# Performance work log

Measured on AMD Instinct MI355X. Metric: run time of the kernel, lower is better.

The kernel has to match this reference:

```python
import jax, jax.numpy as jnp
import numpy as np

B, CD, GD, F, H = 8192, 512, 512, 1024, 8
HD = F // H
EPS = 1e-5  # torch LayerNorm default


def _layernorm(x, g, b):
    m = x.mean(-1, keepdims=True)
    v = ((x - m) ** 2).mean(-1, keepdims=True)
    return (x - m) / jnp.sqrt(v + EPS) * g + b


def setup_inputs() -> dict:
    key = jax.random.key(0)
    ks = jax.random.split(key, 24)
    s = lambda fan_in: 1.0 / np.sqrt(fan_in)
    return {
        "cnn_embed": jax.random.normal(ks[0], (B, CD), jnp.float32),
        "gnn_embed": jax.random.normal(ks[1], (B, GD), jnp.float32),
        # projections (torch Linear: y = x @ W.T + b)
        "cnn_w": jax.random.normal(ks[2], (F, CD), jnp.float32) * s(CD),
        "cnn_b": jax.random.normal(ks[3], (F,), jnp.float32) * s(CD),
        "gnn_w": jax.random.normal(ks[4], (F, GD), jnp.float32) * s(GD),
        "gnn_b": jax.random.normal(ks[5], (F,), jnp.float32) * s(GD),
        # layernorms
        "ln1_g": jnp.ones((F,), jnp.float32),
        "ln1_b": jnp.zeros((F,), jnp.float32),
        "ln2_g": jnp.ones((F,), jnp.float32),
        "ln2_b": jnp.zeros((F,), jnp.float32),
        # MultiheadAttention packed in-proj + out-proj
        "attn_in_w": jax.random.normal(ks[6], (3 * F, F), jnp.float32) * s(F),
        "attn_in_b": jnp.zeros((3 * F,), jnp.float32),
        "attn_out_w": jax.random.normal(ks[7], (F, F), jnp.float32) * s(F),
        "attn_out_b": jnp.zeros((F,), jnp.float32),
        # gate MLP: Linear(2F->F) GELU Linear(F->2) Softmax
        "gate_w1": jax.random.normal(ks[8], (F, 2 * F), jnp.float32) * s(2 * F),
        "gate_b1": jnp.zeros((F,), jnp.float32),
        "gate_w2": jax.random.normal(ks[9], (2, F), jnp.float32) * s(F),
        "gate_b2": jnp.zeros((2,), jnp.float32),
        # out_proj: Linear(F->F) GELU (dropout is identity in eval)
        "proj_w": jax.random.normal(ks[10], (F, F), jnp.float32) * s(F),
        "proj_b": jnp.zeros((F,), jnp.float32),
    }


def reference(cnn_embed, gnn_embed, cnn_w, cnn_b, gnn_w, gnn_b,
              ln1_g, ln1_b, ln2_g, ln2_b,
              attn_in_w, attn_in_b, attn_out_w, attn_out_b,
              gate_w1, gate_b1, gate_w2, gate_b2, proj_w, proj_b):
    c = _layernorm(cnn_embed @ cnn_w.T + cnn_b, ln1_g, ln1_b)  # [B,F]
    g = _layernorm(gnn_embed @ gnn_w.T + gnn_b, ln2_g, ln2_b)  # [B,F]
    combined = jnp.stack([c, g], axis=1)  # [B,2,F]

    # self-attention over the 2-token "sequence" (q=k=v=combined)
    qkv = combined @ attn_in_w.T + attn_in_b  # [B,2,3F]
    q, k, v = jnp.split(qkv, 3, axis=-1)
    split_heads = lambda t: t.reshape(B, 2, H, HD).transpose(0, 2, 1, 3)  # [B,H,2,HD]
    q, k, v = split_heads(q), split_heads(k), split_heads(v)
    scores = jnp.einsum("bhqd,bhkd->bhqk", q, k) / np.sqrt(HD)  # [B,H,2,2]
    attn = jax.nn.softmax(scores, axis=-1)
    o = jnp.einsum("bhqk,bhkd->bhqd", attn, v)  # [B,H,2,HD]
    o = o.transpose(0, 2, 1, 3).reshape(B, 2, F)
    attn_out = o @ attn_out_w.T + attn_out_b  # [B,2,F]

    c_attn = attn_out[:, 0]
    g_attn = attn_out[:, 1]
    gate_in = jnp.concatenate([c_attn, g_attn], axis=-1)  # [B,2F]
    gate_h = jax.nn.gelu(gate_in @ gate_w1.T + gate_b1, approximate=False)
    gate_weights = jax.nn.softmax(gate_h @ gate_w2.T + gate_b2, axis=-1)  # [B,2]

    fused = gate_weights[:, 0:1] * c_attn + gate_weights[:, 1:2] * g_attn
    fused = jax.nn.gelu(fused @ proj_w.T + proj_b, approximate=False)  # dropout=eval identity
    return fused, gate_weights
```

## Files before the change

kernel.cpp:

```cpp
#include <hip/hip_runtime.h>
#include <hip/hip_bf16.h>
#include <math.h>

typedef short short8 __attribute__((ext_vector_type(8)));
typedef float floatx4 __attribute__((ext_vector_type(4)));

__device__ __forceinline__ float bf2f(ushort u) {
    union { unsigned int i; float f; } v; v.i = ((unsigned int)u) << 16; return v.f;
}
__device__ __forceinline__ ushort f2bf(float f) {
    union { float f; unsigned int i; } v; v.f = f;
    unsigned int x = v.i;
    unsigned int lsb = (x >> 16) & 1u;
    x += 0x7fffu + lsb;
    return (ushort)(x >> 16);
}
__device__ __forceinline__ float gelu_f(float x) {
    return 0.5f * x * (1.0f + erff(x * 0.7071067811865475f));
}
__device__ __forceinline__ void store4(ushort* p, float a, float b, float c, float d) {
    ushort4 o; o.x = f2bf(a); o.y = f2bf(b); o.z = f2bf(c); o.w = f2bf(d);
    *(ushort4*)p = o;
}
__device__ __forceinline__ void store4(float* p, float a, float b, float c, float d) {
    *(float4*)p = make_float4(a, b, c, d);
}

struct CvtDesc {
    const float* in[8];
    ushort* out[8];
    int nblk[8];
};
__global__ __launch_bounds__(256) void cvt_all_kernel(CvtDesc d) {
    int b = blockIdx.x;
    int s = 0;
    int off = b;
    while (off >= d.nblk[s]) { off -= d.nblk[s]; s++; }
    int i = off * 1024 + threadIdx.x * 4;
    float4 v = *(const float4*)(d.in[s] + i);
    ushort4 o;
    o.x = f2bf(v.x); o.y = f2bf(v.y); o.z = f2bf(v.z); o.w = f2bf(v.w);
    *(ushort4*)(d.out[s] + i) = o;
}

template<int ACT, typename TOUT>
__global__ __launch_bounds__(256) void gemm_bt(const ushort* __restrict__ A, int lda,
                                               const ushort* __restrict__ W,
                                               const float* __restrict__ bias,
                                               TOUT* __restrict__ C, int ldc,
                                               int M, int N, int K) {
    __shared__ ushort lsA[128 * 32];
    __shared__ ushort lsB[128 * 32];
    const int t = threadIdx.x;
    const int w = t >> 6, l = t & 63;
    const int q = l >> 4, r16 = l & 15;
    const int wm = (w >> 1) * 64, wn = (w & 1) * 64;
    const int m0 = blockIdx.y * 128, n0 = blockIdx.x * 128;

    floatx4 acc[4][4];
#pragma unroll
    for (int i = 0; i < 4; i++)
#pragma unroll
        for (int j = 0; j < 4; j++) acc[i][j] = (floatx4){0.f, 0.f, 0.f, 0.f};

    const int kc = (t & 3) * 8;

    for (int kt = 0; kt < K; kt += 32) {
        __syncthreads();
#pragma unroll
        for (int rr = 0; rr < 2; ++rr) {
            int c = rr * 256 + t;
            int row = c >> 2;
            const ushort* ga = A + (size_t)(m0 + row) * lda + kt + kc;
            const ushort* gb = W + (size_t)(n0 + row) * K + kt + kc;
            __builtin_amdgcn_global_load_lds((const __attribute__((address_space(1))) void*)ga,
                                             (__attribute__((address_space(3))) void*)&lsA[c * 8],
                                             16, 0, 0);
            __builtin_amdgcn_global_load_lds((const __attribute__((address_space(1))) void*)gb,
                                             (__attribute__((address_space(3))) void*)&lsB[c * 8],
                                             16, 0, 0);
        }
        __syncthreads();
        short8 af[4], bfr[4];
#pragma unroll
        for (int i = 0; i < 4; i++) af[i]  = *(const short8*)&lsA[(wm + i * 16 + r16) * 32 + q * 8];
#pragma unroll
        for (int j = 0; j < 4; j++) bfr[j] = *(const short8*)&lsB[(wn + j * 16 + r16) * 32 + q * 8];
#pragma unroll
        for (int i = 0; i < 4; i++)
#pragma unroll
            for (int j = 0; j < 4; j++)
                acc[i][j] = __builtin_amdgcn_mfma_f32_16x16x32_bf16(bfr[j], af[i], acc[i][j], 0, 0, 0);
    }

#pragma unroll
    for (int j = 0; j < 4; j++) {
        const int col = n0 + wn + j * 16 + q * 4;
        const float4 bv = *(const float4*)(bias + col);
#pragma unroll
        for (int i = 0; i < 4; i++) {
            const int row = m0 + wm + i * 16 + r16;
            float v0 = acc[i][j][0] + bv.x;
            float v1 = acc[i][j][1] + bv.y;
            float v2 = acc[i][j][2] + bv.z;
            float v3 = acc[i][j][3] + bv.w;
            if (ACT == 1) { v0 = gelu_f(v0); v1 = gelu_f(v1); v2 = gelu_f(v2); v3 = gelu_f(v3); }
            store4(&C[(size_t)row * ldc + col], v0, v1, v2, v3);
        }
    }
}

__global__ __launch_bounds__(256) void ln_kernel(ushort* __restrict__ comb,
                                                 const float* __restrict__ g1, const float* __restrict__ b1,
                                                 const float* __restrict__ g2, const float* __restrict__ b2) {
    int row = blockIdx.x;
    int s = row & 1;
    const float* g = s ? g2 : g1;
    const float* bb = s ? b2 : b1;
    ushort* p = comb + (size_t)row * 1024;
    int t = threadIdx.x;
    ushort4 u = *(const ushort4*)(p + t * 4);
    float x0 = bf2f(u.x), x1 = bf2f(u.y), x2 = bf2f(u.z), x3 = bf2f(u.w);
    float sum = x0 + x1 + x2 + x3;
    float ss = x0 * x0 + x1 * x1 + x2 * x2 + x3 * x3;
#pragma unroll
    for (int off = 32; off; off >>= 1) {
        sum += __shfl_xor(sum, off);
        ss  += __shfl_xor(ss, off);
    }
    __shared__ float sm[8];
    int wv = t >> 6, l = t & 63;
    if (l == 0) { sm[wv * 2] = sum; sm[wv * 2 + 1] = ss; }
    __syncthreads();
    sum = sm[0] + sm[2] + sm[4] + sm[6];
    ss  = sm[1] + sm[3] + sm[5] + sm[7];
    float mean = sum * (1.0f / 1024.0f);
    float var  = ss * (1.0f / 1024.0f) - mean * mean;
    float rstd = rsqrtf(var + 1e-5f);
    float4 gv = *(const float4*)(g + t * 4);
    float4 bv = *(const float4*)(bb + t * 4);
    ushort4 o;
    o.x = f2bf((x0 - mean) * rstd * gv.x + bv.x);
    o.y = f2bf((x1 - mean) * rstd * gv.y + bv.y);
    o.z = f2bf((x2 - mean) * rstd * gv.z + bv.z);
    o.w = f2bf((x3 - mean) * rstd * gv.w + bv.w);
    *(ushort4*)(p + t * 4) = o;
}

__global__ __launch_bounds__(256) void attn_kernel(ushort* __restrict__ qkv) {
    int wid = blockIdx.x * 4 + (threadIdx.x >> 6);
    int l = threadIdx.x & 63;
    int b = wid >> 3, h = wid & 7;
    ushort* base0 = qkv + (size_t)(b * 2) * 3072 + h * 128 + 2 * l;
    ushort* base1 = base0 + 3072;
    ushort2 uq0 = *(const ushort2*)(base0);
    ushort2 uq1 = *(const ushort2*)(base1);
    ushort2 uk0 = *(const ushort2*)(base0 + 1024);
    ushort2 uk1 = *(const ushort2*)(base1 + 1024);
    ushort2 uv0 = *(const ushort2*)(base0 + 2048);
    ushort2 uv1 = *(const ushort2*)(base1 + 2048);
    float q0a = bf2f(uq0.x), q0b = bf2f(uq0.y);
    float q1a = bf2f(uq1.x), q1b = bf2f(uq1.y);
    float k0a = bf2f(uk0.x), k0b = bf2f(uk0.y);
    float k1a = bf2f(uk1.x), k1b = bf2f(uk1.y);
    float v0a = bf2f(uv0.x), v0b = bf2f(uv0.y);
    float v1a = bf2f(uv1.x), v1b = bf2f(uv1.y);
    float p00 = q0a * k0a + q0b * k0b;
    float p01 = q0a * k1a + q0b * k1b;
    float p10 = q1a * k0a + q1b * k0b;
    float p11 = q1a * k1a + q1b * k1b;
#pragma unroll
    for (int off = 32; off; off >>= 1) {
        p00 += __shfl_xor(p00, off);
        p01 += __shfl_xor(p01, off);
        p10 += __shfl_xor(p10, off);
        p11 += __shfl_xor(p11, off);
    }
    const float sc = 0.08838834764831845f;
    p00 *= sc; p01 *= sc; p10 *= sc; p11 *= sc;
    float m0 = fmaxf(p00, p01), m1 = fmaxf(p10, p11);
    float e00 = expf(p00 - m0), e01 = expf(p01 - m0);
    float e10 = expf(p10 - m1), e11 = expf(p11 - m1);
    float i0 = 1.0f / (e00 + e01), i1 = 1.0f / (e10 + e11);
    float a00 = e00 * i0, a01 = e01 * i0;
    float a10 = e10 * i1, a11 = e11 * i1;
    ushort2 o0, o1;
    o0.x = f2bf(a00 * v0a + a01 * v1a);
    o0.y = f2bf(a00 * v0b + a01 * v1b);
    o1.x = f2bf(a10 * v0a + a11 * v1a);
    o1.y = f2bf(a10 * v0b + a11 * v1b);
    *(ushort2*)(base0) = o0;
    *(ushort2*)(base1) = o1;
}

__global__ __launch_bounds__(256) void gate2_kernel(const ushort* __restrict__ gate_h,
                                                    const float* __restrict__ w2, const float* __restrict__ b2,
                                                    const ushort* __restrict__ attn_out,
                                                    ushort* __restrict__ fused_pre,
                                                    float* __restrict__ gw_out) {
    int b = blockIdx.x;
    int t = threadIdx.x;
    const ushort* hp = gate_h + (size_t)b * 1024;
    ushort4 u = *(const ushort4*)(hp + t * 4);
    float4 w0 = *(const float4*)(w2 + t * 4);
    float4 w1 = *(const float4*)(w2 + 1024 + t * 4);
    float h0 = bf2f(u.x), h1 = bf2f(u.y), h2 = bf2f(u.z), h3 = bf2f(u.w);
    float p0 = h0 * w0.x + h1 * w0.y + h2 * w0.z + h3 * w0.w;
    float p1 = h0 * w1.x + h1 * w1.y + h2 * w1.z + h3 * w1.w;
#pragma unroll
    for (int off = 32; off; off >>= 1) {
        p0 += __shfl_xor(p0, off);
        p1 += __shfl_xor(p1, off);
    }
    __shared__ float sm[8];
    __shared__ float sgw[2];
    int wv = t >> 6, l = t & 63;
    if (l == 0) { sm[wv * 2] = p0; sm[wv * 2 + 1] = p1; }
    __syncthreads();
    if (t == 0) {
        float d0 = sm[0] + sm[2] + sm[4] + sm[6] + b2[0];
        float d1 = sm[1] + sm[3] + sm[5] + sm[7] + b2[1];
        float mx = fmaxf(d0, d1);
        float e0 = expf(d0 - mx), e1 = expf(d1 - mx);
        float inv = 1.0f / (e0 + e1);
        sgw[0] = e0 * inv; sgw[1] = e1 * inv;
        gw_out[b * 2] = e0 * inv;
        gw_out[b * 2 + 1] = e1 * inv;
    }
    __syncthreads();
    float g0 = sgw[0], g1 = sgw[1];
    const ushort* ca = attn_out + (size_t)b * 2048;
    ushort* fp = fused_pre + (size_t)b * 1024;
    ushort4 uc = *(const ushort4*)(ca + t * 4);
    ushort4 ug = *(const ushort4*)(ca + 1024 + t * 4);
    ushort4 o;
    o.x = f2bf(g0 * bf2f(uc.x) + g1 * bf2f(ug.x));
    o.y = f2bf(g0 * bf2f(uc.y) + g1 * bf2f(ug.y));
    o.z = f2bf(g0 * bf2f(uc.z) + g1 * bf2f(ug.z));
    o.w = f2bf(g0 * bf2f(uc.w) + g1 * bf2f(ug.w));
    *(ushort4*)(fp + t * 4) = o;
}

#define OFF_A_CNN  0u
#define OFF_A_GNN  8388608u
#define OFF_W_CNN  16777216u
#define OFF_W_GNN  17825792u
#define OFF_W_QKV  18874368u
#define OFF_W_AO   25165824u
#define OFF_W_G1   27262976u
#define OFF_W_PJ   31457280u
#define OFF_COMB   33554432u
#define OFF_QKV    67108864u
#define OFF_AO     167772160u

extern "C" void kernel_launch(void* const* d_in, const int* in_sizes, int n_in,
                              void* d_out, int out_size, void* d_ws, size_t ws_size,
                              hipStream_t stream) {
    const float* cnn_embed  = (const float*)d_in[0];
    const float* gnn_embed  = (const float*)d_in[1];
    const float* cnn_w      = (const float*)d_in[2];
    const float* cnn_b      = (const float*)d_in[3];
    const float* gnn_w      = (const float*)d_in[4];
    const float* gnn_b      = (const float*)d_in[5];
    const float* ln1_g      = (const float*)d_in[6];
    const float* ln1_b      = (const float*)d_in[7];
    const float* ln2_g      = (const float*)d_in[8];
    const float* ln2_b      = (const float*)d_in[9];
    const float* attn_in_w  = (const float*)d_in[10];
    const float* attn_in_b  = (const float*)d_in[11];
    const float* attn_out_w = (const float*)d_in[12];
    const float* attn_out_b = (const float*)d_in[13];
    const float* gate_w1    = (const float*)d_in[14];
    const float* gate_b1    = (const float*)d_in[15];
    const float* gate_w2    = (const float*)d_in[16];
    const float* gate_b2    = (const float*)d_in[17];
    const float* proj_w     = (const float*)d_in[18];
    const float* proj_b     = (const float*)d_in[19];

    char* ws = (char*)d_ws;
    ushort* a_cnn  = (ushort*)(ws + OFF_A_CNN);
    ushort* a_gnn  = (ushort*)(ws + OFF_A_GNN);
    ushort* w_cnn  = (ushort*)(ws + OFF_W_CNN);
    ushort* w_gnn  = (ushort*)(ws + OFF_W_GNN);
    ushort* w_qkv  = (ushort*)(ws + OFF_W_QKV);
    ushort* w_ao   = (ushort*)(ws + OFF_W_AO);
    ushort* w_g1   = (ushort*)(ws + OFF_W_G1);
    ushort* w_pj   = (ushort*)(ws + OFF_W_PJ);
    ushort* comb   = (ushort*)(ws + OFF_COMB);
    ushort* qkv    = (ushort*)(ws + OFF_QKV);
    ushort* ao     = (ushort*)(ws + OFF_AO);
    ushort* gate_h    = (ushort*)(ws + OFF_COMB);
    ushort* fused_pre = (ushort*)(ws + OFF_COMB + 16777216u);

    float* out_f  = (float*)d_out;
    float* gw_out = out_f + 8192 * 1024;

    CvtDesc cd;
    cd.in[0] = cnn_embed;  cd.out[0] = a_cnn; cd.nblk[0] = 4096;
    cd.in[1] = gnn_embed;  cd.out[1] = a_gnn; cd.nblk[1] = 4096;
    cd.in[2] = cnn_w;      cd.out[2] = w_cnn; cd.nblk[2] = 512;
    cd.in[3] = gnn_w;      cd.out[3] = w_gnn; cd.nblk[3] = 512;
    cd.in[4] = attn_in_w;  cd.out[4] = w_qkv; cd.nblk[4] = 3072;
    cd.in[5] = attn_out_w; cd.out[5] = w_ao;  cd.nblk[5] = 1024;
    cd.in[6] = gate_w1;    cd.out[6] = w_g1;  cd.nblk[6] = 2048;
    cd.in[7] = proj_w;     cd.out[7] = w_pj;  cd.nblk[7] = 1024;
    cvt_all_kernel<<<16384, 256, 0, stream>>>(cd);

    dim3 blk(256);
    dim3 g_embed(1024 / 128, 8192 / 128);
    gemm_bt<0, ushort><<<g_embed, blk, 0, stream>>>(a_cnn, 512, w_cnn, cnn_b, comb, 2048, 8192, 1024, 512);
    gemm_bt<0, ushort><<<g_embed, blk, 0, stream>>>(a_gnn, 512, w_gnn, gnn_b, comb + 1024, 2048, 8192, 1024, 512);

    ln_kernel<<<16384, blk, 0, stream>>>(comb, ln1_g, ln1_b, ln2_g, ln2_b);

    dim3 g_qkv(3072 / 128, 16384 / 128);
    gemm_bt<0, ushort><<<g_qkv, blk, 0, stream>>>(comb, 1024, w_qkv, attn_in_b, qkv, 3072, 16384, 3072, 1024);

    attn_kernel<<<16384, blk, 0, stream>>>(qkv);

    dim3 g_ao(1024 / 128, 16384 / 128);
    gemm_bt<0, ushort><<<g_ao, blk, 0, stream>>>(qkv, 3072, w_ao, attn_out_b, ao, 1024, 16384, 1024, 1024);

    dim3 g_g1(1024 / 128, 8192 / 128);
    gemm_bt<1, ushort><<<g_g1, blk, 0, stream>>>(ao, 2048, w_g1, gate_b1, gate_h, 1024, 8192, 1024, 2048);

    gate2_kernel<<<8192, blk, 0, stream>>>(gate_h, gate_w2, gate_b2, ao, fused_pre, gw_out);

    dim3 g_pj(1024 / 128, 8192 / 128);
    gemm_bt<1, float><<<g_pj, blk, 0, stream>>>(fused_pre, 1024, w_pj, proj_b, out_f, 1024, 8192, 1024, 1024);
}
```

Baseline: 545.4 us.

## Widen GEMM K-tile to 64 with XOR-swizzled LDS and fuse embed conversion

The GEMM core now stages 64-wide K tiles with an XOR swizzle on the LDS column index, meant to cut bank conflicts and halve the number of barrier pairs per K loop. The fp32 embeddings are no longer pre-converted. A new embed_gemm kernel reads them directly, converts to bf16 while filling LDS, and handles both projections in one launch using blockIdx.z. Launch bounds now request 3 blocks per CU. The trade-off is that LDS per block doubles, and the fp32 A path uses plain register loads instead of async global-to-LDS copies.

```diff
diff --git a/kernel.cpp b/kernel.cpp
--- a/kernel.cpp
+++ b/kernel.cpp
@@ -3,6 +3,7 @@
 #include <math.h>
 
 typedef short short8 __attribute__((ext_vector_type(8)));
+typedef ushort ushort8v __attribute__((ext_vector_type(8)));
 typedef float floatx4 __attribute__((ext_vector_type(4)));
 
 __device__ __forceinline__ float bf2f(ushort u) {
@@ -27,9 +28,9 @@
 }
 
 struct CvtDesc {
-    const float* in[8];
-    ushort* out[8];
-    int nblk[8];
+    const float* in[6];
+    ushort* out[6];
+    int nblk[6];
 };
 __global__ __launch_bounds__(256) void cvt_all_kernel(CvtDesc d) {
     int b = blockIdx.x;
@@ -43,19 +44,18 @@
     *(ushort4*)(d.out[s] + i) = o;
 }
 
-template<int ACT, typename TOUT>
-__global__ __launch_bounds__(256) void gemm_bt(const ushort* __restrict__ A, int lda,
-                                               const ushort* __restrict__ W,
-                                               const float* __restrict__ bias,
-                                               TOUT* __restrict__ C, int ldc,
-                                               int M, int N, int K) {
-    __shared__ ushort lsA[128 * 32];
-    __shared__ ushort lsB[128 * 32];
+template<int ACT, int AF32, typename TOUT>
+__device__ __forceinline__ void gemm_core(const void* __restrict__ Av, int lda,
+                                          const ushort* __restrict__ W,
+                                          const float* __restrict__ bias,
+                                          TOUT* __restrict__ C, int ldc,
+                                          int K, int m0, int n0) {
+    __shared__ ushort lsA[128 * 64];
+    __shared__ ushort lsB[128 * 64];
     const int t = threadIdx.x;
     const int w = t >> 6, l = t & 63;
     const int q = l >> 4, r16 = l & 15;
     const int wm = (w >> 1) * 64, wn = (w & 1) * 64;
-    const int m0 = blockIdx.y * 128, n0 = blockIdx.x * 128;
 
     floatx4 acc[4][4];
 #pragma unroll
@@ -63,34 +63,59 @@
 #pragma unroll
         for (int j = 0; j < 4; j++) acc[i][j] = (floatx4){0.f, 0.f, 0.f, 0.f};
 
-    const int kc = (t & 3) * 8;
-
-    for (int kt = 0; kt < K; kt += 32) {
+    const int srow = t >> 3;
+    const int lc   = t & 7;
+    const int s7 = r16 & 7;
+    const int e0 = ((q)     ^ s7) * 8;
+    const int e1 = ((q + 4) ^ s7) * 8;
+
+    for (int kt = 0; kt < K; kt += 64) {
         __syncthreads();
 #pragma unroll
-        for (int rr = 0; rr < 2; ++rr) {
-            int c = rr * 256 + t;
-            int row = c >> 2;
-            const ushort* ga = A + (size_t)(m0 + row) * lda + kt + kc;
-            const ushort* gb = W + (size_t)(n0 + row) * K + kt + kc;
-            __builtin_amdgcn_global_load_lds((const __attribute__((address_space(1))) void*)ga,
-                                             (__attribute__((address_space(3))) void*)&lsA[c * 8],
+        for (int rr = 0; rr < 4; ++rr) {
+            const int row = rr * 32 + srow;
+            const int gc  = (lc ^ (row & 7)) * 8;
+            const ushort* gb = W + (size_t)(n0 + row) * K + kt + gc;
+            __builtin_amdgcn_global_load_lds((const __attribute__((address_space(1))) void*)gb,
+                                             (__attribute__((address_space(3))) void*)&lsB[row * 64 + lc * 8],
                                              16, 0, 0);
-            __builtin_amdgcn_global_load_lds((const __attribute__((address_space(1))) void*)gb,
-                                             (__attribute__((address_space(3))) void*)&lsB[c * 8],
-                                             16, 0, 0);
+            if (!AF32) {
+                const ushort* ga = (const ushort*)Av + (size_t)(m0 + row) * lda + kt + gc;
+                __builtin_amdgcn_global_load_lds((const __attribute__((address_space(1))) void*)ga,
+                                                 (__attribute__((address_space(3))) void*)&lsA[row * 64 + lc * 8],
+                                                 16, 0, 0);
+            } else {
+                const float* ga = (const float*)Av + (size_t)(m0 + row) * lda + kt + gc;
+                float4 f0 = *(const float4*)ga;
+                float4 f1 = *(const float4*)(ga + 4);
+                ushort8v u;
+                u[0] = f2bf(f0.x); u[1] = f2bf(f0.y); u[2] = f2bf(f0.z); u[3] = f2bf(f0.w);
+                u[4] = f2bf(f1.x); u[5] = f2bf(f1.y); u[6] = f2bf(f1.z); u[7] = f2bf(f1.w);
+                *(ushort8v*)&lsA[row * 64 + lc * 8] = u;
+            }
         }
         __syncthreads();
-        short8 af[4], bfr[4];
-#pragma unroll
-        for (int i = 0; i < 4; i++) af[i]  = *(const short8*)&lsA[(wm + i * 16 + r16) * 32 + q * 8];
-#pragma unroll
-        for (int j = 0; j < 4; j++) bfr[j] = *(const short8*)&lsB[(wn + j * 16 + r16) * 32 + q * 8];
-#pragma unroll
-        for (int i = 0; i < 4; i++)
-#pragma unroll
-            for (int j = 0; j < 4; j++)
-                acc[i][j] = __builtin_amdgcn_mfma_f32_16x16x32_bf16(bfr[j], af[i], acc[i][j], 0, 0, 0);
+        {
+            short8 af[4], bfr[4];
+#pragma unroll
+            for (int i = 0; i < 4; i++) af[i]  = *(const short8*)&lsA[(wm + i * 16 + r16) * 64 + e0];
+#pragma unroll
+            for (int j = 0; j < 4; j++) bfr[j] = *(const short8*)&lsB[(wn + j * 16 + r16) * 64 + e0];
+#pragma unroll
+            for (int i = 0; i < 4; i++)
+#pragma unroll
+                for (int j = 0; j < 4; j++)
+                    acc[i][j] = __builtin_amdgcn_mfma_f32_16x16x32_bf16(bfr[j], af[i], acc[i][j], 0, 0, 0);
+#pragma unroll
+            for (int i = 0; i < 4; i++) af[i]  = *(const short8*)&lsA[(wm + i * 16 + r16) * 64 + e1];
+#pragma unroll
+            for (int j = 0; j < 4; j++) bfr[j] = *(const short8*)&lsB[(wn + j * 16 + r16) * 64 + e1];
+#pragma unroll
+            for (int i = 0; i < 4; i++)
+#pragma unroll
+                for (int j = 0; j < 4; j++)
+                    acc[i][j] = __builtin_amdgcn_mfma_f32_16x16x32_bf16(bfr[j], af[i], acc[i][j], 0, 0, 0);
+        }
     }
 
 #pragma unroll
@@ -108,6 +133,28 @@
             store4(&C[(size_t)row * ldc + col], v0, v1, v2, v3);
         }
     }
+}
+
+template<int ACT, typename TOUT>
+__global__ __launch_bounds__(256, 3) void gemm_bt(const ushort* __restrict__ A, int lda,
+                                                  const ushort* __restrict__ W,
+                                                  const float* __restrict__ bias,
+                                                  TOUT* __restrict__ C, int ldc, int K) {
+    gemm_core<ACT, 0, TOUT>(A, lda, W, bias, C, ldc, K, blockIdx.y * 128, blockIdx.x * 128);
+}
+
+__global__ __launch_bounds__(256, 3) void embed_gemm(const float* __restrict__ A0,
+                                                     const float* __restrict__ A1,
+                                                     const ushort* __restrict__ W0,
+                                                     const ushort* __restrict__ W1,
+                                                     const float* __restrict__ b0,
+                                                     const float* __restrict__ b1,
+                                                     ushort* __restrict__ C) {
+    const int z = blockIdx.z;
+    gemm_core<0, 1, ushort>(z ? (const void*)A1 : (const void*)A0, 512,
+                            z ? W1 : W0, z ? b1 : b0,
+                            C + z * 1024, 2048, 512,
+                            blockIdx.y * 128, blockIdx.x * 128);
 }
 
 __global__ __launch_bounds__(256) void ln_kernel(ushort* __restrict__ comb,
@@ -241,8 +288,6 @@
     *(ushort4*)(fp + t * 4) = o;
 }
 
-#define OFF_A_CNN  0u
-#define OFF_A_GNN  8388608u
 #define OFF_W_CNN  16777216u
 #define OFF_W_GNN  17825792u
 #define OFF_W_QKV  18874368u
@@ -278,8 +323,6 @@
     const float* proj_b     = (const float*)d_in[19];
 
     char* ws = (char*)d_ws;
-    ushort* a_cnn  = (ushort*)(ws + OFF_A_CNN);
-    ushort* a_gnn  = (ushort*)(ws + OFF_A_GNN);
     ushort* w_cnn  = (ushort*)(ws + OFF_W_CNN);
     ushort* w_gnn  = (ushort*)(ws + OFF_W_GNN);
     ushort* w_qkv  = (ushort*)(ws + OFF_W_QKV);
@@ -296,36 +339,34 @@
     float* gw_out = out_f + 8192 * 1024;
 
     CvtDesc cd;
-    cd.in[0] = cnn_embed;  cd.out[0] = a_cnn; cd.nblk[0] = 4096;
-    cd.in[1] = gnn_embed;  cd.out[1] = a_gnn; cd.nblk[1] = 4096;
-    cd.in[2] = cnn_w;      cd.out[2] = w_cnn; cd.nblk[2] = 512;
-    cd.in[3] = gnn_w;      cd.out[3] = w_gnn; cd.nblk[3] = 512;
-    cd.in[4] = attn_in_w;  cd.out[4] = w_qkv; cd.nblk[4] = 3072;
-    cd.in[5] = attn_out_w; cd.out[5] = w_ao;  cd.nblk[5] = 1024;
-    cd.in[6] = gate_w1;    cd.out[6] = w_g1;  cd.nblk[6] = 2048;
-    cd.in[7] = proj_w;     cd.out[7] = w_pj;  cd.nblk[7] = 1024;
-    cvt_all_kernel<<<16384, 256, 0, stream>>>(cd);
+    cd.in[0] = cnn_w;      cd.out[0] = w_cnn; cd.nblk[0] = 512;
+    cd.in[1] = gnn_w;      cd.out[1] = w_gnn; cd.nblk[1] = 512;
+    cd.in[2] = attn_in_w;  cd.out[2] = w_qkv; cd.nblk[2] = 3072;
+    cd.in[3] = attn_out_w; cd.out[3] = w_ao;  cd.nblk[3] = 1024;
+    cd.in[4] = gate_w1;    cd.out[4] = w_g1;  cd.nblk[4] = 2048;
+    cd.in[5] = proj_w;     cd.out[5] = w_pj;  cd.nblk[5] = 1024;
+    cvt_all_kernel<<<8192, 256, 0, stream>>>(cd);
 
     dim3 blk(256);
-    dim3 g_embed(1024 / 128, 8192 / 128);
-    gemm_bt<0, ushort><<<g_embed, blk, 0, stream>>>(a_cnn, 512, w_cnn, cnn_b, comb, 2048, 8192, 1024, 512);
-    gemm_bt<0, ushort><<<g_embed, blk, 0, stream>>>(a_gnn, 512, w_gnn, gnn_b, comb + 1024, 2048, 8192, 1024, 512);
+
+    dim3 g_embed(1024 / 128, 8192 / 128, 2);
+    embed_gemm<<<g_embed, blk, 0, stream>>>(cnn_embed, gnn_embed, w_cnn, w_gnn, cnn_b, gnn_b, comb);
 
     ln_kernel<<<16384, blk, 0, stream>>>(comb, ln1_g, ln1_b, ln2_g, ln2_b);
 
     dim3 g_qkv(3072 / 128, 16384 / 128);
-    gemm_bt<0, ushort><<<g_qkv, blk, 0, stream>>>(comb, 1024, w_qkv, attn_in_b, qkv, 3072, 16384, 3072, 1024);
+    gemm_bt<0, ushort><<<g_qkv, blk, 0, stream>>>(comb, 1024, w_qkv, attn_in_b, qkv, 3072, 1024);
 
     attn_kernel<<<16384, blk, 0, stream>>>(qkv);
 
     dim3 g_ao(1024 / 128, 16384 / 128);
-    gemm_bt<0, ushort><<<g_ao, blk, 0, stream>>>(qkv, 3072, w_ao, attn_out_b, ao, 1024, 16384, 1024, 1024);
+    gemm_bt<0, ushort><<<g_ao, blk, 0, stream>>>(qkv, 3072, w_ao, attn_out_b, ao, 1024, 1024);
 
     dim3 g_g1(1024 / 128, 8192 / 128);
-    gemm_bt<1, ushort><<<g_g1, blk, 0, stream>>>(ao, 2048, w_g1, gate_b1, gate_h, 1024, 8192, 1024, 2048);
+    gemm_bt<1, ushort><<<g_g1, blk, 0, stream>>>(ao, 2048, w_g1, gate_b1, gate_h, 1024, 2048);
 
     gate2_kernel<<<8192, blk, 0, stream>>>(gate_h, gate_w2, gate_b2, ao, fused_pre, gw_out);
 
     dim3 g_pj(1024 / 128, 8192 / 128);
-    gemm_bt<1, float><<<g_pj, blk, 0, stream>>>(fused_pre, 1024, w_pj, proj_b, out_f, 1024, 8192, 1024, 1024);
-}
+    gemm_bt<1, float><<<g_pj, blk, 0, stream>>>(fused_pre, 1024, w_pj, proj_b, out_f, 1024, 1024);
+}
```

Result: faster. 504.4 us (-7.5%).
